# Performance work log

Hardware: AMD Instinct MI355X
Metric: run time of the kernel (lower is better)

## Reference

```python
import jax, jax.numpy as jnp
import numpy as np
from jax import lax

TOPK = 5
NUM_CLUSTERS = 10
MAX_ITERS = 10


def setup_inputs() -> dict:
    key = jax.random.key(0)
    k1, k2, k3 = jax.random.split(key, 3)
    B, S, D, K = 8, 4096, 256, 1024
    x = jax.random.normal(k1, (B, S, D), dtype=jnp.float32)
    memory = jax.random.normal(k2, (K, D), dtype=jnp.float32)
    init_idx = jax.random.randint(k3, (B, NUM_CLUSTERS), 0, S, dtype=jnp.int32)
    return {"x": x, "memory": memory, "init_idx": init_idx}


def reference(x, memory, init_idx):
    B, S, D = x.shape
    # --- memory bank retrieval ---
    sim = jnp.einsum('bsd,kd->bsk', x, memory)            # [B,S,K]
    _, topk_idx = lax.top_k(sim, TOPK)                    # [B,S,TOPK]
    memory_ctx = memory[topk_idx]                         # [B,S,TOPK,D]
    attn = jax.nn.softmax(jnp.einsum('bsd,bstd->bst', x, memory_ctx), axis=-1)
    x_enh = x + jnp.einsum('bst,bstd->bsd', attn, memory_ctx)  # [B,S,D]

    # --- in-place k-means ---
    centroids0 = jnp.take_along_axis(x_enh, init_idx[:, :, None], axis=1)  # [B,k,D]
    x_norm_sq = jnp.sum(x_enh ** 2, axis=-1, keepdims=True)                # [B,S,1]

    def step(cent, _):
        dots = jnp.einsum('bsd,bkd->bsk', x_enh, cent)                     # [B,S,k]
        c_norm_sq = jnp.sum(cent ** 2, axis=-1)                            # [B,k]
        dist = x_norm_sq - 2.0 * dots + c_norm_sq[:, None, :]              # [B,S,k]
        assign = jnp.argmin(dist, axis=-1)                                 # [B,S]
        onehot = jax.nn.one_hot(assign, NUM_CLUSTERS, dtype=x_enh.dtype)   # [B,S,k]
        sums = jnp.einsum('bsk,bsd->bkd', onehot, x_enh)                   # [B,k,D]
        counts = jnp.sum(onehot, axis=1)[:, :, None]                       # [B,k,1]
        new_cent = sums / (counts + 1e-8)
        return new_cent, assign

    cent, assigns = lax.scan(step, centroids0, None, length=MAX_ITERS)
    assign = assigns[-1]  # assignments from last iteration (pre final update, as in torch)
    idx = jnp.broadcast_to(assign[:, :, None], (B, S, D))
    quantized = jnp.take_along_axis(cent, idx, axis=1)  # [B,S,D]
    return quantized
```

## Files before the change

### kernel.cpp

```cpp
#include <hip/hip_runtime.h>
#include <math.h>

#define NC 10
#define KITERS 10

#define SWZ(row, q) ((q) ^ (((row) >> 2) & 15))

extern __shared__ float4 lds4[];
__global__ __launch_bounds__(256, 1) void k_enh(const float* __restrict__ x,
                                                const float* __restrict__ mem,
                                                float* __restrict__ xenh) {
  float4* xt = lds4;
  float4* mt = lds4 + 4096;
  float* cv = (float*)lds4;
  int*   ck = (int*)lds4 + 5120;
  float* av = (float*)lds4 + 10240;
  int*   ak = (int*)lds4 + 10560;

  const int tid = threadIdx.x;
  const int tg = tid >> 4;
  const int kg = tid & 15;
  const int tokenBase = blockIdx.x * 64;

  {
    const float4* xg = (const float4*)(x + (size_t)tokenBase * 256);
    const float4* mg = (const float4*)mem;
#pragma unroll
    for (int i = 0; i < 16; ++i) {
      const int p = tid + 256 * i;
      const int row = p >> 6, q = p & 63;
      xt[row * 64 + SWZ(row, q)] = xg[p];
      mt[row * 64 + SWZ(row, q)] = mg[p];
    }
  }
  __syncthreads();

  float t5v[4][5]; int t5k[4][5];
#pragma unroll
  for (int i = 0; i < 4; ++i)
#pragma unroll
    for (int r = 0; r < 5; ++r) { t5v[i][r] = -INFINITY; t5k[i][r] = 0; }

  for (int kc = 0; kc < 16; ++kc) {
    float4 st[16];
    if (kc < 15) {
      const float4* mg = (const float4*)mem + (size_t)(kc + 1) * 4096;
#pragma unroll
      for (int i = 0; i < 16; ++i) st[i] = mg[tid + 256 * i];
    }

    float4 acc[4][4];
#pragma unroll
    for (int i = 0; i < 4; ++i)
#pragma unroll
      for (int j = 0; j < 4; ++j) acc[i][j] = make_float4(0.f, 0.f, 0.f, 0.f);

#pragma unroll 4
    for (int q = 0; q < 64; ++q) {
      float4 mv[4], xv[4];
#pragma unroll
      for (int j = 0; j < 4; ++j) {
        const int row = 4 * kg + j;
        mv[j] = mt[row * 64 + SWZ(row, q)];
      }
#pragma unroll
      for (int i = 0; i < 4; ++i) {
        const int row = 4 * tg + i;
        xv[i] = xt[row * 64 + SWZ(row, q)];
      }
#pragma unroll
      for (int i = 0; i < 4; ++i)
#pragma unroll
        for (int j = 0; j < 4; ++j) {
          acc[i][j].x = __fadd_rn(acc[i][j].x, __fmul_rn(xv[i].x, mv[j].x));
          acc[i][j].y = __fadd_rn(acc[i][j].y, __fmul_rn(xv[i].y, mv[j].y));
          acc[i][j].z = __fadd_rn(acc[i][j].z, __fmul_rn(xv[i].z, mv[j].z));
          acc[i][j].w = __fadd_rn(acc[i][j].w, __fmul_rn(xv[i].w, mv[j].w));
        }
    }

#pragma unroll
    for (int i = 0; i < 4; ++i)
#pragma unroll
      for (int j = 0; j < 4; ++j) {
        const float v = __fadd_rn(__fadd_rn(acc[i][j].x, acc[i][j].z),
                                  __fadd_rn(acc[i][j].y, acc[i][j].w));
        const int kk = kc * 64 + 4 * kg + j;
        if (v > t5v[i][4]) {
          t5v[i][4] = v; t5k[i][4] = kk;
          if (t5v[i][4] > t5v[i][3]) { float a = t5v[i][3]; t5v[i][3] = t5v[i][4]; t5v[i][4] = a; int ia = t5k[i][3]; t5k[i][3] = t5k[i][4]; t5k[i][4] = ia; }
          if (t5v[i][3] > t5v[i][2]) { float a = t5v[i][2]; t5v[i][2] = t5v[i][3]; t5v[i][3] = a; int ia = t5k[i][2]; t5k[i][2] = t5k[i][3]; t5k[i][3] = ia; }
          if (t5v[i][2] > t5v[i][1]) { float a = t5v[i][1]; t5v[i][1] = t5v[i][2]; t5v[i][2] = a; int ia = t5k[i][1]; t5k[i][1] = t5k[i][2]; t5k[i][2] = ia; }
          if (t5v[i][1] > t5v[i][0]) { float a = t5v[i][0]; t5v[i][0] = t5v[i][1]; t5v[i][1] = a; int ia = t5k[i][0]; t5k[i][0] = t5k[i][1]; t5k[i][1] = ia; }
        }
      }

    __syncthreads();
    if (kc < 15) {
#pragma unroll
      for (int i = 0; i < 16; ++i) {
        const int p = tid + 256 * i;
        const int row = p >> 6, q = p & 63;
        mt[row * 64 + SWZ(row, q)] = st[i];
      }
      __syncthreads();
    }
  }
  __syncthreads();

#pragma unroll
  for (int i = 0; i < 4; ++i) {
    const int token = 4 * tg + i;
#pragma unroll
    for (int r = 0; r < 5; ++r) {
      cv[token * 80 + kg * 5 + r] = t5v[i][r];
      ck[token * 80 + kg * 5 + r] = t5k[i][r];
    }
  }
  __syncthreads();

  if (tid < 64) {
    const int token = tid;
    float tv[5]; int tk[5];
#pragma unroll
    for (int r = 0; r < 5; ++r) {
      float best = -INFINITY; int bi = 0, bk = 0x7fffffff;
      for (int c = 0; c < 80; ++c) {
        const float vv = cv[token * 80 + c]; const int kkc = ck[token * 80 + c];
        if (vv > best || (vv == best && kkc < bk)) { best = vv; bi = c; bk = kkc; }
      }
      tv[r] = best; tk[r] = bk; cv[token * 80 + bi] = -INFINITY;
    }
    float mx = tv[0];
#pragma unroll
    for (int r = 1; r < 5; ++r) mx = fmaxf(mx, tv[r]);
    float e[5];
#pragma unroll
    for (int r = 0; r < 5; ++r)
      e[r] = (float)exp((double)__fsub_rn(tv[r], mx));
    float s = e[0];
#pragma unroll
    for (int r = 1; r < 5; ++r) s = __fadd_rn(s, e[r]);
#pragma unroll
    for (int r = 0; r < 5; ++r) { av[token * 5 + r] = __fdiv_rn(e[r], s); ak[token * 5 + r] = tk[r]; }
  }
  __syncthreads();

#pragma unroll
  for (int i = 0; i < 16; ++i) {
    const int flat = tid + 256 * i;
    const int token = flat >> 6, q = flat & 63;
    const float a0 = av[token * 5 + 0], a1 = av[token * 5 + 1], a2 = av[token * 5 + 2],
                a3 = av[token * 5 + 3], a4 = av[token * 5 + 4];
    const float4 xv = ((const float4*)(x + (size_t)(tokenBase + token) * 256))[q];
    const float4 m0 = ((const float4*)(mem + (size_t)ak[token * 5 + 0] * 256))[q];
    const float4 m1 = ((const float4*)(mem + (size_t)ak[token * 5 + 1] * 256))[q];
    const float4 m2 = ((const float4*)(mem + (size_t)ak[token * 5 + 2] * 256))[q];
    const float4 m3 = ((const float4*)(mem + (size_t)ak[token * 5 + 3] * 256))[q];
    const float4 m4 = ((const float4*)(mem + (size_t)ak[token * 5 + 4] * 256))[q];
    float4 o;
    {
      float ctx = __fmul_rn(a0, m0.x);
      ctx = __fadd_rn(ctx, __fmul_rn(a1, m1.x));
      ctx = __fadd_rn(ctx, __fmul_rn(a2, m2.x));
      ctx = __fadd_rn(ctx, __fmul_rn(a3, m3.x));
      ctx = __fadd_rn(ctx, __fmul_rn(a4, m4.x));
      o.x = __fadd_rn(xv.x, ctx);
    }
    {
      float ctx = __fmul_rn(a0, m0.y);
      ctx = __fadd_rn(ctx, __fmul_rn(a1, m1.y));
      ctx = __fadd_rn(ctx, __fmul_rn(a2, m2.y));
      ctx = __fadd_rn(ctx, __fmul_rn(a3, m3.y));
      ctx = __fadd_rn(ctx, __fmul_rn(a4, m4.y));
      o.y = __fadd_rn(xv.y, ctx);
    }
    {
      float ctx = __fmul_rn(a0, m0.z);
      ctx = __fadd_rn(ctx, __fmul_rn(a1, m1.z));
      ctx = __fadd_rn(ctx, __fmul_rn(a2, m2.z));
      ctx = __fadd_rn(ctx, __fmul_rn(a3, m3.z));
      ctx = __fadd_rn(ctx, __fmul_rn(a4, m4.z));
      o.z = __fadd_rn(xv.z, ctx);
    }
    {
      float ctx = __fmul_rn(a0, m0.w);
      ctx = __fadd_rn(ctx, __fmul_rn(a1, m1.w));
      ctx = __fadd_rn(ctx, __fmul_rn(a2, m2.w));
      ctx = __fadd_rn(ctx, __fmul_rn(a3, m3.w));
      ctx = __fadd_rn(ctx, __fmul_rn(a4, m4.w));
      o.w = __fadd_rn(xv.w, ctx);
    }
    ((float4*)(xenh + (size_t)tokenBase * 256))[flat] = o;
  }
}

__global__ __launch_bounds__(256) void k_zero(int* __restrict__ p, int n) {
  const int i = blockIdx.x * 256 + threadIdx.x;
  if (i < n) p[i] = 0;
}

__global__ __launch_bounds__(64) void k_init(const float* __restrict__ xenh,
                                             const int* __restrict__ init_idx,
                                             float* __restrict__ cent) {
  const int i = blockIdx.x;
  const int b = i / NC;
  const int s = init_idx[i];
  const int l = threadIdx.x;
  ((float4*)(cent + (size_t)i * 256))[l] =
      ((const float4*)(xenh + ((size_t)b * 4096 + s) * 256))[l];
}

__global__ __launch_bounds__(256) void k_assign(const float* __restrict__ xenh,
                                                const float* __restrict__ cent,
                                                int* __restrict__ assign,
                                                int* __restrict__ cnt) {
  __shared__ float cl[NC * 256];
  const int tid = threadIdx.x;
  const int b = blockIdx.x & 7;
  const int j = blockIdx.x >> 3;
  const int tokenBase = b * 4096 + j * 128;
  for (int i = tid; i < NC * 256; i += 256)
    cl[i] = cent[(size_t)b * NC * 256 + i];
  __syncthreads();

  const int token = tokenBase + (tid >> 1);
  const int h = tid & 1;
  const float4* px4 = (const float4*)(xenh + (size_t)token * 256 + h * 128);
  const float* pc = cl + h * 128;

  float r[NC][8];
  float4 c0 = px4[0], c1 = px4[1];
#pragma unroll
  for (int ib = 0; ib < 16; ++ib) {
    float4 n0, n1;
    if (ib < 15) { n0 = px4[2 * ib + 2]; n1 = px4[2 * ib + 3]; }
    const float p8[8] = {c0.x, c0.y, c0.z, c0.w, c1.x, c1.y, c1.z, c1.w};
    const int i = ib * 8;
    if (ib == 0) {
#pragma unroll
      for (int k = 0; k < NC; ++k)
#pragma unroll
        for (int jj = 0; jj < 8; ++jj) {
          const float d = __fsub_rn(p8[jj], pc[k * 256 + jj]);
          r[k][jj] = __fmul_rn(d, d);
        }
    } else {
#pragma unroll
      for (int k = 0; k < NC; ++k)
#pragma unroll
        for (int jj = 0; jj < 8; ++jj) {
          const float d = __fsub_rn(p8[jj], pc[k * 256 + i + jj]);
          r[k][jj] = __fadd_rn(r[k][jj], __fmul_rn(d, d));
        }
    }
    c0 = n0; c1 = n1;
  }

  float best = INFINITY; int bk = 0;
#pragma unroll
  for (int k = 0; k < NC; ++k) {
    const float blkOwn =
        __fadd_rn(__fadd_rn(__fadd_rn(r[k][0], r[k][1]), __fadd_rn(r[k][2], r[k][3])),
                  __fadd_rn(__fadd_rn(r[k][4], r[k][5]), __fadd_rn(r[k][6], r[k][7])));
    const float blkOther = __shfl_xor(blkOwn, 1);
    const float dist = __fadd_rn(blkOwn, blkOther);
    if (dist < best) { best = dist; bk = k; }
  }
  if (h == 0) assign[token] = bk;
#pragma unroll
  for (int k = 0; k < NC; ++k) {
    const unsigned long long m =
        __ballot(bk == k) & 0x5555555555555555ULL;
    if ((tid & 63) == 0) atomicAdd(&cnt[b * NC + k], (int)__popcll(m));
  }
}

__global__ __launch_bounds__(64) void k_sums(const float* __restrict__ xenh,
                                             const int* __restrict__ assign,
                                             const int* __restrict__ cnt,
                                             float* __restrict__ cent) {
  const int b = blockIdx.x & 7;
  const int rem = blockIdx.x >> 3;
  const int k = rem >> 2;
  const int d = (rem & 3) * 64 + threadIdx.x;
  const float* xb = xenh + (size_t)b * 4096 * 256 + d;
  const int* ab = assign + b * 4096;

  float acc = 0.0f;
  for (int c = 0; c < 64; ++c) {
    float xe[64]; int ar[64];
#pragma unroll
    for (int j = 0; j < 64; ++j) xe[j] = xb[(size_t)(c * 64 + j) * 256];
#pragma unroll
    for (int j = 0; j < 64; ++j) ar[j] = ab[c * 64 + j];
#pragma unroll
    for (int j = 0; j < 64; ++j)
      acc = __fadd_rn(acc, (ar[j] == k) ? xe[j] : 0.0f);
  }
  const int cc = cnt[b * NC + k];
  cent[((size_t)(b * NC + k)) * 256 + d] = (cc == 0) ? 0.0f : __fdiv_rn(acc, (float)cc);
}

__global__ __launch_bounds__(256) void k_quant(const float* __restrict__ cent,
                                               const int* __restrict__ assign,
                                               float* __restrict__ out) {
  const int token = blockIdx.x * 4 + (threadIdx.x >> 6);
  const int l = threadIdx.x & 63;
  const int b = token >> 12;
  const int a = assign[token];
  ((float4*)out)[(size_t)token * 64 + l] =
      ((const float4*)cent)[(size_t)(b * NC + a) * 64 + l];
}

extern "C" void kernel_launch(void* const* d_in, const int* in_sizes, int n_in,
                              void* d_out, int out_size, void* d_ws, size_t ws_size,
                              hipStream_t stream) {
  const float* x = (const float*)d_in[0];
  const float* mem = (const float*)d_in[1];
  const int* init_idx = (const int*)d_in[2];
  float* xenh = (float*)d_out;
  char* ws = (char*)d_ws;

  float* cent   = (float*)(ws);
  int*   assign = (int*)  (ws + 81920);
  int*   cntbuf = (int*)  (ws + 212992);

  (void)hipFuncSetAttribute((const void*)k_enh,
                            hipFuncAttributeMaxDynamicSharedMemorySize, 131072);

  k_zero<<<4, 256, 0, stream>>>(cntbuf, KITERS * 8 * NC);
  k_enh<<<512, 256, 131072, stream>>>(x, mem, xenh);
  k_init<<<80, 64, 0, stream>>>(xenh, init_idx, cent);
  for (int it = 0; it < KITERS; ++it) {
    k_assign<<<256, 256, 0, stream>>>(xenh, cent, assign, cntbuf + it * 8 * NC);
    k_sums<<<320, 64, 0, stream>>>(xenh, assign, cntbuf + it * 8 * NC, cent);
  }
  k_quant<<<8192, 256, 0, stream>>>(cent, assign, (float*)d_out);
}
```

Before: 1.826 ms.

## Transpose enhanced activations once so centroid sums read contiguous float4 rows

Adds a one-time transpose of x_enh into a [B,D,S] workspace buffer. A new k_sums_T kernel then streams each feature dimension contiguously with float4 and int4 loads instead of doing strided scalar loads per token. The k_assign prefetch is also deepened to two stages. The trade-off is an extra 32MB transpose pass and workspace use, and the new path runs only when the workspace is large enough.

```diff
diff --git a/kernel.cpp b/kernel.cpp
--- a/kernel.cpp
+++ b/kernel.cpp
@@ -195,6 +195,22 @@
   }
 }
 
+__global__ __launch_bounds__(256) void k_transpose_x(const float* __restrict__ in,
+                                                     float* __restrict__ outT) {
+  __shared__ float t[32][33];
+  const int tx = threadIdx.x & 31, ty = threadIdx.x >> 5;
+  const int s0 = blockIdx.x * 32, d0 = blockIdx.y * 32, b = blockIdx.z;
+  const float* ib = in + (size_t)b * 4096 * 256;
+  float* ob = outT + (size_t)b * 256 * 4096;
+#pragma unroll
+  for (int i = 0; i < 4; ++i)
+    t[ty + 8 * i][tx] = ib[(size_t)(s0 + ty + 8 * i) * 256 + d0 + tx];
+  __syncthreads();
+#pragma unroll
+  for (int i = 0; i < 4; ++i)
+    ob[(size_t)(d0 + ty + 8 * i) * 4096 + s0 + tx] = t[tx][ty + 8 * i];
+}
+
 __global__ __launch_bounds__(256) void k_zero(int* __restrict__ p, int n) {
   const int i = blockIdx.x * 256 + threadIdx.x;
   if (i < n) p[i] = 0;
@@ -231,10 +247,11 @@
 
   float r[NC][8];
   float4 c0 = px4[0], c1 = px4[1];
+  float4 d0_ = px4[2], d1_ = px4[3];
 #pragma unroll
   for (int ib = 0; ib < 16; ++ib) {
-    float4 n0, n1;
-    if (ib < 15) { n0 = px4[2 * ib + 2]; n1 = px4[2 * ib + 3]; }
+    float4 e0, e1;
+    if (ib < 14) { e0 = px4[2 * ib + 4]; e1 = px4[2 * ib + 5]; }
     const float p8[8] = {c0.x, c0.y, c0.z, c0.w, c1.x, c1.y, c1.z, c1.w};
     const int i = ib * 8;
     if (ib == 0) {
@@ -254,7 +271,7 @@
           r[k][jj] = __fadd_rn(r[k][jj], __fmul_rn(d, d));
         }
     }
-    c0 = n0; c1 = n1;
+    c0 = d0_; c1 = d1_; d0_ = e0; d1_ = e1;
   }
 
   float best = INFINITY; int bk = 0;
@@ -274,6 +291,36 @@
         __ballot(bk == k) & 0x5555555555555555ULL;
     if ((tid & 63) == 0) atomicAdd(&cnt[b * NC + k], (int)__popcll(m));
   }
+}
+
+__global__ __launch_bounds__(64) void k_sums_T(const float* __restrict__ xT,
+                                               const int* __restrict__ assign,
+                                               const int* __restrict__ cnt,
+                                               float* __restrict__ cent) {
+  const int b = blockIdx.x & 7;
+  const int rem = blockIdx.x >> 3;
+  const int k = rem >> 2;
+  const int d = (rem & 3) * 64 + threadIdx.x;
+  const float4* xc = (const float4*)(xT + ((size_t)b * 256 + d) * 4096);
+  const int4* ac = (const int4*)(assign + b * 4096);
+
+  float acc = 0.0f;
+  for (int c = 0; c < 64; ++c) {
+    float4 xe[16]; int4 ar[16];
+#pragma unroll
+    for (int j = 0; j < 16; ++j) xe[j] = xc[c * 16 + j];
+#pragma unroll
+    for (int j = 0; j < 16; ++j) ar[j] = ac[c * 16 + j];
+#pragma unroll
+    for (int j = 0; j < 16; ++j) {
+      acc = __fadd_rn(acc, (ar[j].x == k) ? xe[j].x : 0.0f);
+      acc = __fadd_rn(acc, (ar[j].y == k) ? xe[j].y : 0.0f);
+      acc = __fadd_rn(acc, (ar[j].z == k) ? xe[j].z : 0.0f);
+      acc = __fadd_rn(acc, (ar[j].w == k) ? xe[j].w : 0.0f);
+    }
+  }
+  const int cc = cnt[b * NC + k];
+  cent[((size_t)(b * NC + k)) * 256 + d] = (cc == 0) ? 0.0f : __fdiv_rn(acc, (float)cc);
 }
 
 __global__ __launch_bounds__(64) void k_sums(const float* __restrict__ xenh,
@@ -325,16 +372,22 @@
   float* cent   = (float*)(ws);
   int*   assign = (int*)  (ws + 81920);
   int*   cntbuf = (int*)  (ws + 212992);
+  float* xT     = (float*)(ws + (1 << 20));
+  const bool useT = ws_size >= ((size_t)34 << 20);
 
   (void)hipFuncSetAttribute((const void*)k_enh,
                             hipFuncAttributeMaxDynamicSharedMemorySize, 131072);
 
   k_zero<<<4, 256, 0, stream>>>(cntbuf, KITERS * 8 * NC);
   k_enh<<<512, 256, 131072, stream>>>(x, mem, xenh);
+  if (useT) k_transpose_x<<<dim3(128, 8, 8), 256, 0, stream>>>(xenh, xT);
   k_init<<<80, 64, 0, stream>>>(xenh, init_idx, cent);
   for (int it = 0; it < KITERS; ++it) {
     k_assign<<<256, 256, 0, stream>>>(xenh, cent, assign, cntbuf + it * 8 * NC);
-    k_sums<<<320, 64, 0, stream>>>(xenh, assign, cntbuf + it * 8 * NC, cent);
+    if (useT)
+      k_sums_T<<<320, 64, 0, stream>>>(xT, assign, cntbuf + it * 8 * NC, cent);
+    else
+      k_sums<<<320, 64, 0, stream>>>(xenh, assign, cntbuf + it * 8 * NC, cent);
   }
   k_quant<<<8192, 256, 0, stream>>>(cent, assign, (float*)d_out);
 }
```

Result: faster. 1.775 ms (-2.8%).
